# Optimization experiments

Hardware: AMD Instinct MI355X
Metric: run time of the kernel (lower is better)

The kernel has to match this reference:

```python
import jax, jax.numpy as jnp
import numpy as np

# ---- static config (mirrors init_kwargs) ----
B, N, C_IN, C_OUT = 4, 8192, 128, 256
RATIO = 0.25
M = int(N * RATIO)          # sampled centers per cloud (fps ratio)
RADIUS = 0.1
MAX_NN = 64                 # max_num_neighbors
K = 16                      # num kernel points
D_MID = C_IN // 2           # pre_mlp: in_features -> in_features // 2
KP_EXTENT = RADIUS          # kernel-point influence extent (linear influence)


def setup_inputs() -> dict:
    key = jax.random.key(0)
    ks = jax.random.split(key, 10)
    x = jax.random.normal(ks[0], (B, N, C_IN), jnp.float32)
    pos = jax.random.uniform(ks[1], (B, N, 3), jnp.float32)  # unit cube
    W_pre = jax.random.normal(ks[2], (C_IN, D_MID), jnp.float32) / np.sqrt(C_IN).astype(np.float32)
    b_pre = jnp.zeros((D_MID,), jnp.float32)
    kp_pos = jax.random.normal(ks[3], (K, 3), jnp.float32) * (0.3 * RADIUS)
    kp_W = jax.random.normal(ks[4], (K, D_MID, D_MID), jnp.float32) / np.sqrt(D_MID * K).astype(np.float32)
    W_post = jax.random.normal(ks[5], (D_MID, C_OUT), jnp.float32) / np.sqrt(D_MID).astype(np.float32)
    b_post = jnp.zeros((C_OUT,), jnp.float32)
    W_sc = jax.random.normal(ks[6], (C_IN, C_OUT), jnp.float32) / np.sqrt(C_IN).astype(np.float32)
    b_sc = jnp.zeros((C_OUT,), jnp.float32)
    return dict(x=x, pos=pos, W_pre=W_pre, b_pre=b_pre, kp_pos=kp_pos, kp_W=kp_W,
                W_post=W_post, b_post=b_post, W_sc=W_sc, b_sc=b_sc)


def _fps(p):
    """Farthest point sampling on one cloud p:[N,3] -> idx:[M] (start at point 0)."""
    mind = jnp.sum((p - p[0]) ** 2, axis=-1)  # [N]
    def step(mind, _):
        i = jnp.argmax(mind).astype(jnp.int32)
        mind = jnp.minimum(mind, jnp.sum((p - p[i]) ** 2, axis=-1))
        return mind, i
    _, rest = jax.lax.scan(step, mind, None, length=M - 1)
    return jnp.concatenate([jnp.zeros((1,), jnp.int32), rest])


def reference(x, pos, W_pre, b_pre, kp_pos, kp_W, W_post, b_post, W_sc, b_sc):
    def _cloud(xb, pb):
        # xb:[N,C_IN], pb:[N,3]
        idx = _fps(pb)                                   # [M]
        centers = pb[idx]                                # [M,3]
        # radius neighbor search: nearest MAX_NN, mask to ball of RADIUS
        d2 = jnp.sum((centers[:, None, :] - pb[None, :, :]) ** 2, axis=-1)   # [M,N]
        neg_d2, nn_idx = jax.lax.top_k(-d2, MAX_NN)      # [M,MAX_NN]
        valid = (-neg_d2) <= RADIUS ** 2                 # [M,MAX_NN]
        # pre mlp then gather neighbor features (x_j)
        x_pre = xb @ W_pre + b_pre                       # [N,D_MID]
        x_j = x_pre[nn_idx]                              # [M,MAX_NN,D_MID]
        # kernel-point conv: linear influence of each kernel point
        rel = pb[nn_idx] - centers[:, None, :]           # [M,MAX_NN,3]
        dist = jnp.sqrt(jnp.sum((rel[:, :, None, :] - kp_pos[None, None, :, :]) ** 2, axis=-1) + 1e-12)  # [M,MAX_NN,K]
        infl = jnp.maximum(1.0 - dist / KP_EXTENT, 0.0) * valid[:, :, None]
        # aggregate (sum over neighbors) per kernel point, then contract with kernel weights
        s = jnp.einsum('mek,med->mkd', infl, x_j)        # [M,K,D_MID]
        feat = jnp.einsum('mkd,kdo->mo', s, kp_W)        # [M,D_MID]
        feat = feat @ W_post + b_post                    # [M,C_OUT]
        short = xb[idx] @ W_sc + b_sc                    # residual shortcut on sampled points
        return feat + short, centers

    out_feat, out_pos = jax.vmap(_cloud)(x, pos)         # [B,M,C_OUT], [B,M,3]
    return out_feat, out_pos
```

## Files before the change

### kernel.cpp

```cpp
#include <hip/hip_runtime.h>

#define B_    4
#define N_    8192
#define CIN   128
#define COUT  256
#define M_    2048
#define K_    16
#define DM    64
#define MAXNN 64
#define CAP   128
#define R2    0.01f
#define EXT   0.1f

typedef float v2f __attribute__((ext_vector_type(2)));
typedef unsigned long long ull;

__device__ __forceinline__ float d2_exact(float ax, float ay, float az,
                                          float bx, float by, float bz) {
    float dx = ax - bx, dy = ay - by, dz = az - bz;
    return __fadd_rn(__fadd_rn(__fmul_rn(dx, dx), __fmul_rn(dy, dy)), __fmul_rn(dz, dz));
}

#define DPP_STEP2(CTRL)                                                                   \
    {                                                                                     \
        unsigned tlo = (unsigned)__builtin_amdgcn_update_dpp(0, (int)klo, CTRL, 0xF, 0xF, true); \
        unsigned thi = (unsigned)__builtin_amdgcn_update_dpp(0, (int)khi, CTRL, 0xF, 0xF, true); \
        unsigned long long tk = ((unsigned long long)thi << 32) | tlo;                    \
        unsigned long long ck = ((unsigned long long)khi << 32) | klo;                    \
        if (tk > ck) { klo = tlo; khi = thi; }                                            \
    }

__global__ __launch_bounds__(512, 2) void fps_pre_kernel(const float* __restrict__ pos,
                                                         int* __restrict__ idx_out,
                                                         float* __restrict__ out_pos,
                                                         const float* __restrict__ x,
                                                         const float* __restrict__ Wp,
                                                         const float* __restrict__ bvec,
                                                         float* __restrict__ xpre) {
    __shared__ union {
        struct { float sx[N_]; float sy[N_]; float sz[N_]; ull slots[2][8]; } f;
        struct { float Ws[CIN * DM]; float xs[32][CIN]; } p;
    } sh;

    const int t = threadIdx.x;

    if (blockIdx.x >= 4) {
        const size_t rowBase = (size_t)(blockIdx.x - 4) * 32;
        for (int i = t; i < CIN * DM; i += 512) sh.p.Ws[i] = Wp[i];
        for (int i = t; i < 32 * CIN; i += 512) {
            int r = i >> 7, c = i & 127;
            sh.p.xs[r][c] = x[(rowBase + r) * CIN + c];
        }
        __syncthreads();
        const int col = t & 63, r0 = t >> 6;
        float acc[4];
        float bias = bvec[col];
#pragma unroll
        for (int rr = 0; rr < 4; rr++) acc[rr] = bias;
        for (int c = 0; c < CIN; c++) {
            float w = sh.p.Ws[c * DM + col];
#pragma unroll
            for (int rr = 0; rr < 4; rr++) acc[rr] = fmaf(sh.p.xs[r0 + 8 * rr][c], w, acc[rr]);
        }
#pragma unroll
        for (int rr = 0; rr < 4; rr++) xpre[(rowBase + r0 + 8 * rr) * DM + col] = acc[rr];
        return;
    }

    const int b = blockIdx.x;
    const float* pb = pos + (size_t)b * N_ * 3;

    v2f px[8], py[8], pz[8], mind[8];
#pragma unroll
    for (int jj = 0; jj < 8; jj++) {
        int n0 = t + (2 * jj) * 512, n1 = n0 + 512;
        float x0 = pb[n0 * 3 + 0], y0 = pb[n0 * 3 + 1], z0 = pb[n0 * 3 + 2];
        float x1 = pb[n1 * 3 + 0], y1 = pb[n1 * 3 + 1], z1 = pb[n1 * 3 + 2];
        px[jj] = (v2f){x0, x1};
        py[jj] = (v2f){y0, y1};
        pz[jj] = (v2f){z0, z1};
        mind[jj] = (v2f){1e30f, 1e30f};
        sh.f.sx[n0] = x0; sh.f.sy[n0] = y0; sh.f.sz[n0] = z0;
        sh.f.sx[n1] = x1; sh.f.sy[n1] = y1; sh.f.sz[n1] = z1;
    }
    float cx = pb[0], cy = pb[1], cz = pb[2];
    if (t == 0) {
        idx_out[b * M_ + 0] = 0;
        float* op = out_pos + ((size_t)(b * M_ + 0)) * 3;
        op[0] = cx; op[1] = cy; op[2] = cz;
    }
    __syncthreads();

    for (int m = 1; m < M_; m++) {
        float bv = -1.0f; int bj = 0;
        {
#pragma clang fp contract(off)
            v2f cx2 = (v2f){cx, cx}, cy2 = (v2f){cy, cy}, cz2 = (v2f){cz, cz};
#pragma unroll
            for (int jj = 0; jj < 8; jj++) {
                v2f dx = px[jj] - cx2, dy = py[jj] - cy2, dz = pz[jj] - cz2;
                v2f d = (dx * dx + dy * dy) + dz * dz;
                v2f mo = mind[jj];
                float n0 = fminf(mo.x, d.x);
                float n1 = fminf(mo.y, d.y);
                mind[jj] = (v2f){n0, n1};
                if (n0 > bv) { bv = n0; bj = 2 * jj; }
                if (n1 > bv) { bv = n1; bj = 2 * jj + 1; }
            }
        }
        const int bn = t + (bj << 9);
        unsigned klo = ~(unsigned)bn;
        unsigned khi = __float_as_uint(bv);

        DPP_STEP2(0x111)
        DPP_STEP2(0x112)
        DPP_STEP2(0x114)
        DPP_STEP2(0x118)
        DPP_STEP2(0x142)
        DPP_STEP2(0x143)

        ull* sl = sh.f.slots[m & 1];
        if ((t & 63) == 63) sl[t >> 6] = ((ull)khi << 32) | klo;
        __syncthreads();

        ull k0 = sl[0], k1 = sl[1], k2 = sl[2], k3 = sl[3];
        ull k4 = sl[4], k5 = sl[5], k6 = sl[6], k7 = sl[7];
        ull a0 = k0 > k1 ? k0 : k1;
        ull a1 = k2 > k3 ? k2 : k3;
        ull a2 = k4 > k5 ? k4 : k5;
        ull a3 = k6 > k7 ? k6 : k7;
        ull b0 = a0 > a1 ? a0 : a1;
        ull b1 = a2 > a3 ? a2 : a3;
        ull kk = b0 > b1 ? b0 : b1;

        const unsigned widx = ~(unsigned)(kk & 0xFFFFFFFFull);
        cx = sh.f.sx[widx]; cy = sh.f.sy[widx]; cz = sh.f.sz[widx];
        if (t == 0) {
            idx_out[b * M_ + m] = (int)widx;
            float* op = out_pos + ((size_t)(b * M_ + m)) * 3;
            op[0] = cx; op[1] = cy; op[2] = cz;
        }
    }
}

__global__ __launch_bounds__(256) void conv_kernel(const float* __restrict__ pos,
                                                   const float* __restrict__ x,
                                                   const float* __restrict__ xpre,
                                                   const int* __restrict__ idxs,
                                                   const float* __restrict__ kp_pos,
                                                   const float* __restrict__ kp_W,
                                                   const float* __restrict__ W_post,
                                                   const float* __restrict__ b_post,
                                                   const float* __restrict__ W_sc,
                                                   const float* __restrict__ b_sc,
                                                   float* __restrict__ out_feat) {
    const int blk = blockIdx.x;
    const int b = blk / M_;
    const int m = blk % M_;
    const int t = threadIdx.x;

    __shared__ int   nIdx[CAP];
    __shared__ float nD2[CAP];
    __shared__ int   cntS;
    __shared__ float infl[MAXNN][K_];
    __shared__ float xj[MAXNN][DM];
    __shared__ float sS[K_ * DM];
    __shared__ float featP[4][DM];
    __shared__ float xg[CIN];

    const float* pb = pos + (size_t)b * N_ * 3;
    const int ctr = idxs[b * M_ + m];
    const float cx = pb[ctr * 3 + 0], cy = pb[ctr * 3 + 1], cz = pb[ctr * 3 + 2];

    if (t == 0) cntS = 0;
    __syncthreads();

    for (int j = 0; j < N_ / 256; j++) {
        int n = j * 256 + t;
        float x0 = pb[n * 3 + 0], y0 = pb[n * 3 + 1], z0 = pb[n * 3 + 2];
        float d = d2_exact(x0, y0, z0, cx, cy, cz);
        if (d <= R2) {
            int p = atomicAdd(&cntS, 1);
            if (p < CAP) { nIdx[p] = n; nD2[p] = d; }
        }
    }
    __syncthreads();
    int cnt = cntS; if (cnt > CAP) cnt = CAP;
    if (cnt > MAXNN) {
        if (t == 0) {
            for (int s = 0; s < MAXNN; s++) {
                int best = s;
                for (int q = s + 1; q < cnt; q++) {
                    if (nD2[q] < nD2[best] || (nD2[q] == nD2[best] && nIdx[q] < nIdx[best])) best = q;
                }
                float td = nD2[best]; nD2[best] = nD2[s]; nD2[s] = td;
                int ti = nIdx[best]; nIdx[best] = nIdx[s]; nIdx[s] = ti;
            }
        }
        __syncthreads();
        cnt = MAXNN;
    }

    if (t < cnt) {
        int n = nIdx[t];
        float rx = pb[n * 3 + 0] - cx, ry = pb[n * 3 + 1] - cy, rz = pb[n * 3 + 2] - cz;
#pragma unroll
        for (int k = 0; k < K_; k++) {
            float dx = rx - kp_pos[k * 3 + 0];
            float dy = ry - kp_pos[k * 3 + 1];
            float dz = rz - kp_pos[k * 3 + 2];
            float dist = sqrtf(dx * dx + dy * dy + dz * dz + 1e-12f);
            infl[t][k] = fmaxf(1.0f - dist / EXT, 0.0f);
        }
    }
    for (int i = t; i < cnt * DM; i += 256) {
        int e = i >> 6, d = i & 63;
        xj[e][d] = xpre[((size_t)b * N_ + nIdx[e]) * DM + d];
    }
    __syncthreads();

#pragma unroll
    for (int p = 0; p < 4; p++) {
        int pair = t + p * 256;
        int k = pair >> 6, d = pair & 63;
        float acc = 0.f;
        for (int e = 0; e < cnt; e++) acc = fmaf(infl[e][k], xj[e][d], acc);
        sS[pair] = acc;
    }
    __syncthreads();

    {
        int dprime = t & 63, ks = t >> 6;
        float acc = 0.f;
        for (int k = ks * 4; k < ks * 4 + 4; k++) {
            const float* kw = kp_W + ((size_t)k * DM) * DM + dprime;
#pragma unroll
            for (int d = 0; d < DM; d++) acc = fmaf(sS[k * DM + d], kw[d * DM], acc);
        }
        featP[ks][dprime] = acc;
    }
    __syncthreads();
    if (t < DM) featP[0][t] = featP[0][t] + featP[1][t] + featP[2][t] + featP[3][t];
    if (t < CIN) xg[t] = x[((size_t)b * N_ + ctr) * CIN + t];
    __syncthreads();

    {
        const int o = t;
        float acc = b_post[o] + b_sc[o];
#pragma unroll 8
        for (int d = 0; d < DM; d++) acc = fmaf(featP[0][d], W_post[d * COUT + o], acc);
#pragma unroll 8
        for (int c = 0; c < CIN; c++) acc = fmaf(xg[c], W_sc[c * COUT + o], acc);
        out_feat[((size_t)(b * M_ + m)) * COUT + o] = acc;
    }
}

extern "C" void kernel_launch(void* const* d_in, const int* in_sizes, int n_in,
                              void* d_out, int out_size, void* d_ws, size_t ws_size,
                              hipStream_t stream) {
    const float* x      = (const float*)d_in[0];
    const float* pos    = (const float*)d_in[1];
    const float* W_pre  = (const float*)d_in[2];
    const float* b_pre  = (const float*)d_in[3];
    const float* kp_pos = (const float*)d_in[4];
    const float* kp_W   = (const float*)d_in[5];
    const float* W_post = (const float*)d_in[6];
    const float* b_post = (const float*)d_in[7];
    const float* W_sc   = (const float*)d_in[8];
    const float* b_sc   = (const float*)d_in[9];

    float* out_feat = (float*)d_out;
    float* out_pos  = (float*)d_out + (size_t)B_ * M_ * COUT;

    int*   idxs = (int*)d_ws;
    float* xpre = (float*)((char*)d_ws + 64 * 1024);

    fps_pre_kernel<<<4 + (B_ * N_) / 32, 512, 0, stream>>>(pos, idxs, out_pos,
                                                           x, W_pre, b_pre, xpre);
    conv_kernel<<<B_ * M_, 256, 0, stream>>>(pos, x, xpre, idxs, kp_pos, kp_W,
                                             W_post, b_post, W_sc, b_sc, out_feat);
}
```

Measured before the change: 2.073 ms.

## Fuse FPS, pre-MLP and conv into one persistent kernel with flag-based streaming

Merges the FPS/pre-MLP kernel and the conv kernel into a single launch. Conv blocks spin on per-cloud progress flags that FPS publishes every 32 centers, plus a counter of finished pre-MLP blocks, so conv work overlaps the long serial FPS loop instead of waiting for it to finish. The risks are spin-wait overhead, deadlock if conv blocks occupy the CUs before FPS blocks are scheduled, and conv blocks now running at 512 threads with half of them idle in the later phases.

```diff
diff --git a/kernel.cpp b/kernel.cpp
--- a/kernel.cpp
+++ b/kernel.cpp
@@ -12,6 +12,10 @@
 #define R2    0.01f
 #define EXT   0.1f
 
+#define NPRE  1024
+#define CONV0 (4 + NPRE)
+#define PUB   32
+
 typedef float v2f __attribute__((ext_vector_type(2)));
 typedef unsigned long long ull;
 
@@ -30,22 +34,141 @@
         if (tk > ck) { klo = tlo; khi = thi; }                                            \
     }
 
-__global__ __launch_bounds__(512, 2) void fps_pre_kernel(const float* __restrict__ pos,
-                                                         int* __restrict__ idx_out,
-                                                         float* __restrict__ out_pos,
-                                                         const float* __restrict__ x,
-                                                         const float* __restrict__ Wp,
-                                                         const float* __restrict__ bvec,
-                                                         float* __restrict__ xpre) {
+__global__ void init_kernel(int* __restrict__ flags) {
+    if (threadIdx.x < 8) flags[threadIdx.x] = 0;
+}
+
+__global__ __launch_bounds__(512, 2) void mega_kernel(const float* __restrict__ pos,
+                                                      int* __restrict__ idx_out,
+                                                      float* __restrict__ out_pos,
+                                                      const float* __restrict__ x,
+                                                      const float* __restrict__ Wp,
+                                                      const float* __restrict__ bvec,
+                                                      float* __restrict__ xpre,
+                                                      const float* __restrict__ kp_pos,
+                                                      const float* __restrict__ kp_W,
+                                                      const float* __restrict__ W_post,
+                                                      const float* __restrict__ b_post,
+                                                      const float* __restrict__ W_sc,
+                                                      const float* __restrict__ b_sc,
+                                                      float* __restrict__ out_feat,
+                                                      int* __restrict__ flags) {
     __shared__ union {
         struct { float sx[N_]; float sy[N_]; float sz[N_]; ull slots[2][8]; } f;
         struct { float Ws[CIN * DM]; float xs[32][CIN]; } p;
+        struct { int nIdx[CAP]; float nD2[CAP]; int cntS;
+                 float infl[MAXNN][K_]; float xj[MAXNN][DM];
+                 float sS[K_ * DM]; float featP[4][DM]; float xg[CIN]; } c;
     } sh;
 
     const int t = threadIdx.x;
-
-    if (blockIdx.x >= 4) {
-        const size_t rowBase = (size_t)(blockIdx.x - 4) * 32;
+    const int blk = blockIdx.x;
+
+    if (blk >= CONV0) {
+        const int cid = blk - CONV0;
+        const int cb = cid & 3;
+        const int cm = cid >> 2;
+
+        if (t == 0) {
+            while (__hip_atomic_load(&flags[cb], __ATOMIC_RELAXED, __HIP_MEMORY_SCOPE_AGENT) <= cm ||
+                   __hip_atomic_load(&flags[4], __ATOMIC_RELAXED, __HIP_MEMORY_SCOPE_AGENT) < NPRE) {
+                __builtin_amdgcn_s_sleep(64);
+            }
+            __threadfence();
+            sh.c.cntS = 0;
+        }
+        __syncthreads();
+
+        const float* pb = pos + (size_t)cb * N_ * 3;
+        const int ctr = idx_out[cb * M_ + cm];
+        const float ccx = pb[ctr * 3 + 0], ccy = pb[ctr * 3 + 1], ccz = pb[ctr * 3 + 2];
+
+        for (int j = 0; j < N_ / 512; j++) {
+            int n = j * 512 + t;
+            float x0 = pb[n * 3 + 0], y0 = pb[n * 3 + 1], z0 = pb[n * 3 + 2];
+            float d = d2_exact(x0, y0, z0, ccx, ccy, ccz);
+            if (d <= R2) {
+                int pp = atomicAdd(&sh.c.cntS, 1);
+                if (pp < CAP) { sh.c.nIdx[pp] = n; sh.c.nD2[pp] = d; }
+            }
+        }
+        __syncthreads();
+        int cnt = sh.c.cntS; if (cnt > CAP) cnt = CAP;
+        if (cnt > MAXNN) {
+            if (t == 0) {
+                for (int s = 0; s < MAXNN; s++) {
+                    int best = s;
+                    for (int q = s + 1; q < cnt; q++) {
+                        if (sh.c.nD2[q] < sh.c.nD2[best] ||
+                            (sh.c.nD2[q] == sh.c.nD2[best] && sh.c.nIdx[q] < sh.c.nIdx[best])) best = q;
+                    }
+                    float td = sh.c.nD2[best]; sh.c.nD2[best] = sh.c.nD2[s]; sh.c.nD2[s] = td;
+                    int ti = sh.c.nIdx[best]; sh.c.nIdx[best] = sh.c.nIdx[s]; sh.c.nIdx[s] = ti;
+                }
+            }
+            __syncthreads();
+            cnt = MAXNN;
+        }
+
+        if (t < cnt) {
+            int n = sh.c.nIdx[t];
+            float rx = pb[n * 3 + 0] - ccx, ry = pb[n * 3 + 1] - ccy, rz = pb[n * 3 + 2] - ccz;
+#pragma unroll
+            for (int k = 0; k < K_; k++) {
+                float dx = rx - kp_pos[k * 3 + 0];
+                float dy = ry - kp_pos[k * 3 + 1];
+                float dz = rz - kp_pos[k * 3 + 2];
+                float dist = sqrtf(dx * dx + dy * dy + dz * dz + 1e-12f);
+                sh.c.infl[t][k] = fmaxf(1.0f - dist / EXT, 0.0f);
+            }
+        }
+        for (int i = t; i < cnt * DM; i += 512) {
+            int e = i >> 6, d = i & 63;
+            sh.c.xj[e][d] = xpre[((size_t)cb * N_ + sh.c.nIdx[e]) * DM + d];
+        }
+        __syncthreads();
+
+        if (t < 256) {
+#pragma unroll
+            for (int p4 = 0; p4 < 4; p4++) {
+                int pair = t + p4 * 256;
+                int k = pair >> 6, d = pair & 63;
+                float acc = 0.f;
+                for (int e = 0; e < cnt; e++) acc = fmaf(sh.c.infl[e][k], sh.c.xj[e][d], acc);
+                sh.c.sS[pair] = acc;
+            }
+        }
+        __syncthreads();
+
+        if (t < 256) {
+            int dprime = t & 63, ks = t >> 6;
+            float acc = 0.f;
+            for (int k = ks * 4; k < ks * 4 + 4; k++) {
+                const float* kw = kp_W + ((size_t)k * DM) * DM + dprime;
+#pragma unroll
+                for (int d = 0; d < DM; d++) acc = fmaf(sh.c.sS[k * DM + d], kw[d * DM], acc);
+            }
+            sh.c.featP[ks][dprime] = acc;
+        }
+        __syncthreads();
+        if (t < DM) sh.c.featP[0][t] = sh.c.featP[0][t] + sh.c.featP[1][t] + sh.c.featP[2][t] + sh.c.featP[3][t];
+        if (t < CIN) sh.c.xg[t] = x[((size_t)cb * N_ + ctr) * CIN + t];
+        __syncthreads();
+
+        if (t < 256) {
+            const int o = t;
+            float acc = b_post[o] + b_sc[o];
+#pragma unroll 8
+            for (int d = 0; d < DM; d++) acc = fmaf(sh.c.featP[0][d], W_post[d * COUT + o], acc);
+#pragma unroll 8
+            for (int cc = 0; cc < CIN; cc++) acc = fmaf(sh.c.xg[cc], W_sc[cc * COUT + o], acc);
+            out_feat[((size_t)(cb * M_ + cm)) * COUT + o] = acc;
+        }
+        return;
+    }
+
+    if (blk >= 4) {
+        const size_t rowBase = (size_t)(blk - 4) * 32;
         for (int i = t; i < CIN * DM; i += 512) sh.p.Ws[i] = Wp[i];
         for (int i = t; i < 32 * CIN; i += 512) {
             int r = i >> 7, c = i & 127;
@@ -64,10 +187,13 @@
         }
 #pragma unroll
         for (int rr = 0; rr < 4; rr++) xpre[(rowBase + r0 + 8 * rr) * DM + col] = acc[rr];
+        __threadfence();
+        __syncthreads();
+        if (t == 0) atomicAdd(&flags[4], 1);
         return;
     }
 
-    const int b = blockIdx.x;
+    const int b = blk;
     const float* pb = pos + (size_t)b * N_ * 3;
 
     v2f px[8], py[8], pz[8], mind[8];
@@ -139,119 +265,11 @@
             idx_out[b * M_ + m] = (int)widx;
             float* op = out_pos + ((size_t)(b * M_ + m)) * 3;
             op[0] = cx; op[1] = cy; op[2] = cz;
-        }
-    }
-}
-
-__global__ __launch_bounds__(256) void conv_kernel(const float* __restrict__ pos,
-                                                   const float* __restrict__ x,
-                                                   const float* __restrict__ xpre,
-                                                   const int* __restrict__ idxs,
-                                                   const float* __restrict__ kp_pos,
-                                                   const float* __restrict__ kp_W,
-                                                   const float* __restrict__ W_post,
-                                                   const float* __restrict__ b_post,
-                                                   const float* __restrict__ W_sc,
-                                                   const float* __restrict__ b_sc,
-                                                   float* __restrict__ out_feat) {
-    const int blk = blockIdx.x;
-    const int b = blk / M_;
-    const int m = blk % M_;
-    const int t = threadIdx.x;
-
-    __shared__ int   nIdx[CAP];
-    __shared__ float nD2[CAP];
-    __shared__ int   cntS;
-    __shared__ float infl[MAXNN][K_];
-    __shared__ float xj[MAXNN][DM];
-    __shared__ float sS[K_ * DM];
-    __shared__ float featP[4][DM];
-    __shared__ float xg[CIN];
-
-    const float* pb = pos + (size_t)b * N_ * 3;
-    const int ctr = idxs[b * M_ + m];
-    const float cx = pb[ctr * 3 + 0], cy = pb[ctr * 3 + 1], cz = pb[ctr * 3 + 2];
-
-    if (t == 0) cntS = 0;
-    __syncthreads();
-
-    for (int j = 0; j < N_ / 256; j++) {
-        int n = j * 256 + t;
-        float x0 = pb[n * 3 + 0], y0 = pb[n * 3 + 1], z0 = pb[n * 3 + 2];
-        float d = d2_exact(x0, y0, z0, cx, cy, cz);
-        if (d <= R2) {
-            int p = atomicAdd(&cntS, 1);
-            if (p < CAP) { nIdx[p] = n; nD2[p] = d; }
-        }
-    }
-    __syncthreads();
-    int cnt = cntS; if (cnt > CAP) cnt = CAP;
-    if (cnt > MAXNN) {
-        if (t == 0) {
-            for (int s = 0; s < MAXNN; s++) {
-                int best = s;
-                for (int q = s + 1; q < cnt; q++) {
-                    if (nD2[q] < nD2[best] || (nD2[q] == nD2[best] && nIdx[q] < nIdx[best])) best = q;
-                }
-                float td = nD2[best]; nD2[best] = nD2[s]; nD2[s] = td;
-                int ti = nIdx[best]; nIdx[best] = nIdx[s]; nIdx[s] = ti;
-            }
-        }
-        __syncthreads();
-        cnt = MAXNN;
-    }
-
-    if (t < cnt) {
-        int n = nIdx[t];
-        float rx = pb[n * 3 + 0] - cx, ry = pb[n * 3 + 1] - cy, rz = pb[n * 3 + 2] - cz;
-#pragma unroll
-        for (int k = 0; k < K_; k++) {
-            float dx = rx - kp_pos[k * 3 + 0];
-            float dy = ry - kp_pos[k * 3 + 1];
-            float dz = rz - kp_pos[k * 3 + 2];
-            float dist = sqrtf(dx * dx + dy * dy + dz * dz + 1e-12f);
-            infl[t][k] = fmaxf(1.0f - dist / EXT, 0.0f);
-        }
-    }
-    for (int i = t; i < cnt * DM; i += 256) {
-        int e = i >> 6, d = i & 63;
-        xj[e][d] = xpre[((size_t)b * N_ + nIdx[e]) * DM + d];
-    }
-    __syncthreads();
-
-#pragma unroll
-    for (int p = 0; p < 4; p++) {
-        int pair = t + p * 256;
-        int k = pair >> 6, d = pair & 63;
-        float acc = 0.f;
-        for (int e = 0; e < cnt; e++) acc = fmaf(infl[e][k], xj[e][d], acc);
-        sS[pair] = acc;
-    }
-    __syncthreads();
-
-    {
-        int dprime = t & 63, ks = t >> 6;
-        float acc = 0.f;
-        for (int k = ks * 4; k < ks * 4 + 4; k++) {
-            const float* kw = kp_W + ((size_t)k * DM) * DM + dprime;
-#pragma unroll
-            for (int d = 0; d < DM; d++) acc = fmaf(sS[k * DM + d], kw[d * DM], acc);
-        }
-        featP[ks][dprime] = acc;
-    }
-    __syncthreads();
-    if (t < DM) featP[0][t] = featP[0][t] + featP[1][t] + featP[2][t] + featP[3][t];
-    if (t < CIN) xg[t] = x[((size_t)b * N_ + ctr) * CIN + t];
-    __syncthreads();
-
-    {
-        const int o = t;
-        float acc = b_post[o] + b_sc[o];
-#pragma unroll 8
-        for (int d = 0; d < DM; d++) acc = fmaf(featP[0][d], W_post[d * COUT + o], acc);
-#pragma unroll 8
-        for (int c = 0; c < CIN; c++) acc = fmaf(xg[c], W_sc[c * COUT + o], acc);
-        out_feat[((size_t)(b * M_ + m)) * COUT + o] = acc;
+            if ((m & (PUB - 1)) == (PUB - 1)) {
+                __threadfence();
+                __hip_atomic_store(&flags[b], m + 1, __ATOMIC_RELAXED, __HIP_MEMORY_SCOPE_AGENT);
+            }
+        }
     }
 }
 
@@ -272,11 +290,13 @@
     float* out_feat = (float*)d_out;
     float* out_pos  = (float*)d_out + (size_t)B_ * M_ * COUT;
 
-    int*   idxs = (int*)d_ws;
-    float* xpre = (float*)((char*)d_ws + 64 * 1024);
-
-    fps_pre_kernel<<<4 + (B_ * N_) / 32, 512, 0, stream>>>(pos, idxs, out_pos,
-                                                           x, W_pre, b_pre, xpre);
-    conv_kernel<<<B_ * M_, 256, 0, stream>>>(pos, x, xpre, idxs, kp_pos, kp_W,
-                                             W_post, b_post, W_sc, b_sc, out_feat);
+    int*   idxs  = (int*)d_ws;
+    int*   flags = (int*)((char*)d_ws + 48 * 1024);
+    float* xpre  = (float*)((char*)d_ws + 64 * 1024);
+
+    init_kernel<<<1, 64, 0, stream>>>(flags);
+    mega_kernel<<<CONV0 + B_ * M_, 512, 0, stream>>>(pos, idxs, out_pos,
+                                                     x, W_pre, b_pre, xpre,
+                                                     kp_pos, kp_W, W_post, b_post,
+                                                     W_sc, b_sc, out_feat, flags);
 }
```

Result: faster. 1.917 ms (median of 3 runs) (-7.5%).
